# Kernel optimization log

Measured on AMD Instinct MI355X. Metric: run time of the kernel, lower is better.

Reference implementation:

```python
import jax, jax.numpy as jnp
import numpy as np

N = 50000   # nodes
E = 800000  # edges per relation (avg degree 16)
IN = 128    # input feature dim
H = 2       # attention heads per layer
OUT = 64    # output feats per head
R = 2       # number of relations
NEG_SLOPE = 0.2


def _edge_softmax(e, dst, n):
    # e: [E, H] edge scores; softmax over incoming edges of each dst node
    m = jax.ops.segment_max(e, dst, num_segments=n)  # [N, H]
    m = jnp.where(jnp.isfinite(m), m, 0.0)
    ex = jnp.exp(e - jax.lax.stop_gradient(m)[dst])
    s = jax.ops.segment_sum(ex, dst, num_segments=n)  # [N, H]
    return ex / s[dst]


def _gat_layer(h, W, al, ar, b, src, dst):
    # h: [N, in]; W: [R, in, H*OUT]; al/ar: [R, H, OUT]; b: [R, H*OUT]
    # src/dst: [R, E] int32. HeteroGraphConv with sum aggregation over relations.
    acc = jnp.zeros((N, H, OUT), h.dtype)
    for r in range(R):  # small fixed relation count
        f = (h @ W[r]).reshape(N, H, OUT)           # projected feats
        el = (f * al[r]).sum(-1)                    # [N, H]
        er = (f * ar[r]).sum(-1)                    # [N, H]
        e = jax.nn.leaky_relu(el[src[r]] + er[dst[r]], NEG_SLOPE)  # [E, H]
        a = _edge_softmax(e, dst[r], N)             # [E, H]
        msg = f[src[r]] * a[:, :, None]             # [E, H, OUT]
        agg = jax.ops.segment_sum(msg, dst[r], num_segments=N)     # [N, H, OUT]
        acc = acc + jax.nn.elu(agg + b[r].reshape(1, H, OUT))
    return acc.reshape(N, H * OUT)  # flatten(1)


def setup_inputs() -> dict:
    key = jax.random.key(0)
    k = jax.random.split(key, 13)
    s = 0.05
    f32 = jnp.float32
    return {
        "x": jax.random.normal(k[0], (N, IN), f32),
        "W0": jax.random.normal(k[1], (R, IN, H * OUT), f32) * s,
        "al0": jax.random.normal(k[2], (R, H, OUT), f32) * s,
        "ar0": jax.random.normal(k[3], (R, H, OUT), f32) * s,
        "b0": jax.random.normal(k[4], (R, H * OUT), f32) * s,
        "W1": jax.random.normal(k[5], (R, H * OUT, H * OUT), f32) * s,
        "al1": jax.random.normal(k[6], (R, H, OUT), f32) * s,
        "ar1": jax.random.normal(k[7], (R, H, OUT), f32) * s,
        "b1": jax.random.normal(k[8], (R, H * OUT), f32) * s,
        "src0": jax.random.randint(k[9], (R, E), 0, N, jnp.int32),
        "dst0": jax.random.randint(k[10], (R, E), 0, N, jnp.int32),
        "src1": jax.random.randint(k[11], (R, E), 0, N, jnp.int32),
        "dst1": jax.random.randint(k[12], (R, E), 0, N, jnp.int32),
    }


def reference(x, W0, al0, ar0, b0, W1, al1, ar1, b1, src0, dst0, src1, dst1):
    h = _gat_layer(x, W0, al0, ar0, b0, src0, dst0)  # [N, H*OUT]
    h = _gat_layer(h, W1, al1, ar1, b1, src1, dst1)  # [N, H*OUT]
    return h
```

## Files before the change

kernel.cpp:

```cpp
#include <hip/hip_runtime.h>

#define NN 50000
#define NE 800000
#define DIM 128
#define NB 128
#define CH 2048
#define CAP 8192
#define MAXDEG 64
#define WINH 196
#define BPSET ((NE + CH - 1) / CH)
#define NBIN_BLOCKS (4 * BPSET)
#define GRBLK ((NN + 63) / 64)
#define NGEMM (2 * GRBLK)

typedef unsigned int uint;
typedef unsigned short ushort;
typedef __attribute__((ext_vector_type(8))) short v8s;
typedef __attribute__((ext_vector_type(4))) float v4f;

__device__ __forceinline__ ushort f2bf(float f) {
    union { float f; uint i; } c; c.f = f;
    const uint r = (c.i + 0x7fffu + ((c.i >> 16) & 1u)) >> 16;
    return (ushort)r;
}

__device__ __forceinline__ void conv_body(
    const float* __restrict__ W0, const float* __restrict__ W1,
    ushort* __restrict__ WT, int bid)
{
    const int t = bid * 256 + threadIdx.x;
#pragma unroll
    for (int i = 0; i < 4; i++) {
        const int o = t * 4 + i;
        const int m = o >> 14, rem = o & 16383;
        const int nrow = rem >> 7, k = rem & 127;
        const float* src = (m < 2) ? (W0 + (size_t)m * 16384)
                                   : (W1 + (size_t)(m - 2) * 16384);
        WT[o] = f2bf(src[k * 128 + nrow]);
    }
}

__device__ __forceinline__ void gemm_rel_body(
    ushort (*tile)[136],
    const ushort* __restrict__ hbf, const float* __restrict__ xf,
    const ushort* __restrict__ WTr,
    const float* __restrict__ alr, const float* __restrict__ arr,
    ushort* __restrict__ fgr, float* __restrict__ elp, float* __restrict__ erp,
    int n, int is_f32, int rb)
{
    const int tid = threadIdx.x;
    const int w = tid >> 6, lane = tid & 63;
    const int quad = lane >> 4, l16 = lane & 15;
    const int row0 = rb * 64 + w * 16;

    int arow = row0 + l16;
    if (arow >= n) arow = n - 1;

    v8s afr[4];
    if (is_f32) {
        const float* ap = xf + (size_t)arow * DIM + quad * 8;
#pragma unroll
        for (int kt = 0; kt < 4; kt++) {
            const float4 a0 = *(const float4*)(ap + kt * 32);
            const float4 a1 = *(const float4*)(ap + kt * 32 + 4);
            ushort tmp[8] = { f2bf(a0.x), f2bf(a0.y), f2bf(a0.z), f2bf(a0.w),
                              f2bf(a1.x), f2bf(a1.y), f2bf(a1.z), f2bf(a1.w) };
            afr[kt] = *(const v8s*)tmp;
        }
    } else {
        const ushort* ap = hbf + (size_t)arow * DIM + quad * 8;
#pragma unroll
        for (int kt = 0; kt < 4; kt++) afr[kt] = *(const v8s*)(ap + kt * 32);
    }

    const ushort* bp = WTr + (size_t)l16 * DIM + quad * 8;
    v4f acc[8];
#pragma unroll
    for (int nt = 0; nt < 8; nt++) acc[nt] = (v4f)0.0f;
#pragma unroll
    for (int kt = 0; kt < 4; kt++) {
#pragma unroll
        for (int nt = 0; nt < 8; nt++) {
            const v8s b = *(const v8s*)(bp + (size_t)nt * 16 * DIM + kt * 32);
            acc[nt] = __builtin_amdgcn_mfma_f32_16x16x32_bf16(afr[kt], b, acc[nt], 0, 0, 0);
        }
    }

    float pel[4][2], per2[4][2];
#pragma unroll
    for (int r = 0; r < 4; r++)
        pel[r][0] = pel[r][1] = per2[r][0] = per2[r][1] = 0.f;
#pragma unroll
    for (int nt = 0; nt < 8; nt++) {
        const int col = nt * 16 + l16;
        const float av = alr[col], rv = arr[col];
        const int head = nt >> 2;
#pragma unroll
        for (int r = 0; r < 4; r++) {
            pel[r][head] += acc[nt][r] * av;
            per2[r][head] += acc[nt][r] * rv;
        }
    }
#pragma unroll
    for (int o = 1; o < 16; o <<= 1) {
#pragma unroll
        for (int r = 0; r < 4; r++) {
#pragma unroll
            for (int h = 0; h < 2; h++) {
                pel[r][h] += __shfl_xor(pel[r][h], o);
                per2[r][h] += __shfl_xor(per2[r][h], o);
            }
        }
    }
    if (l16 == 0) {
#pragma unroll
        for (int r = 0; r < 4; r++) {
            const int row = row0 + quad * 4 + r;
            if (row < n) {
#pragma unroll
                for (int h = 0; h < 2; h++) {
                    elp[row * 2 + h] = pel[r][h];
                    erp[row * 2 + h] = per2[r][h];
                }
            }
        }
    }

    const int lr0 = w * 16 + quad * 4;
#pragma unroll
    for (int nt = 0; nt < 8; nt++) {
        const int col = nt * 16 + l16;
#pragma unroll
        for (int r = 0; r < 4; r++)
            tile[lr0 + r][col] = f2bf(acc[nt][r]);
    }
    __syncthreads();
    const int srow = tid >> 2, ch = tid & 3;
    const int grow = rb * 64 + srow;
    if (grow < n) {
        const uint4* lp = (const uint4*)&tile[srow][ch * 32];
        uint4* gp = (uint4*)(fgr + (size_t)grow * DIM + ch * 32);
        gp[0] = lp[0];
        gp[1] = lp[1];
        gp[2] = lp[2];
        gp[3] = lp[3];
    }
}

__global__ __launch_bounds__(256) void gemm_rel(
    const ushort* __restrict__ hbf, const float* __restrict__ xf,
    const ushort* __restrict__ WT,
    const float* __restrict__ al, const float* __restrict__ ar,
    ushort* __restrict__ fg0, ushort* __restrict__ fg1,
    float* __restrict__ elb, int n, int is_f32)
{
    __shared__ ushort tile[64][136];
    const int rel = blockIdx.x & 1, rb = blockIdx.x >> 1;
    float* elp = elb + (size_t)rel * NN * 4;
    gemm_rel_body(tile, hbf, xf, WT + (size_t)rel * DIM * DIM,
                  al + rel * DIM, ar + rel * DIM,
                  rel ? fg1 : fg0, elp, elp + (size_t)NN * 2,
                  n, is_f32, rb);
}

__device__ __forceinline__ void bin_body(
    char* smem,
    const int* __restrict__ dst0, const int* __restrict__ dst1,
    const int* __restrict__ src0, const int* __restrict__ src1,
    int* __restrict__ gcur, uint* __restrict__ binned, int bid)
{
    int* hist  = (int*)smem;
    int* ebase = hist + NB;
    int* lcur  = ebase + NB;
    int* gbase = lcur + NB;
    int* sc    = gbase + NB;
    uint* stage = (uint*)(sc + NB);

    const int s = bid / BPSET, cb = bid - s * BPSET;
    const int* dstp = (s < 2) ? (dst0 + (size_t)s * NE) : (dst1 + (size_t)(s - 2) * NE);
    const int* srcp = (s < 2) ? (src0 + (size_t)s * NE) : (src1 + (size_t)(s - 2) * NE);
    const int e0 = cb * CH;
    const int t = threadIdx.x;

    if (t < NB) hist[t] = 0;
    __syncthreads();

    int myd[8], mys[8];
#pragma unroll
    for (int k = 0; k < 8; k++) {
        const int e = e0 + t + k * 256;
        if (e < NE) {
            const int d = dstp[e];
            myd[k] = d;
            mys[k] = srcp[e];
            atomicAdd(&hist[(d * NB) / NN], 1);
        } else myd[k] = -1;
    }
    __syncthreads();
    if (t < NB) sc[t] = hist[t];
    __syncthreads();
    for (int o = 1; o < NB; o <<= 1) {
        int tv = 0;
        if (t < NB && t >= o) tv = sc[t - o];
        __syncthreads();
        if (t < NB) sc[t] += tv;
        __syncthreads();
    }
    if (t < NB) {
        ebase[t] = sc[t] - hist[t];
        lcur[t]  = sc[t] - hist[t];
        gbase[t] = (s * NB + t) * CAP + atomicAdd(&gcur[s * NB + t], hist[t]);
    }
    __syncthreads();
#pragma unroll
    for (int k = 0; k < 8; k++) {
        if (myd[k] >= 0) {
            const int b = (myd[k] * NB) / NN;
            const int p = atomicAdd(&lcur[b], 1);
            stage[p] = ((uint)myd[k] << 16) | (uint)mys[k];
        }
    }
    __syncthreads();
    const int total = ebase[NB - 1] + hist[NB - 1];
    for (int i = t; i < total; i += 256) {
        const uint v = stage[i];
        const int b = ((int)(v >> 16) * NB) / NN;
        binned[gbase[b] + (i - ebase[b])] = v;
    }
}

__global__ __launch_bounds__(256) void prep_a(
    const float* __restrict__ W0, const float* __restrict__ W1,
    ushort* __restrict__ WT,
    const int* __restrict__ dst0, const int* __restrict__ dst1,
    const int* __restrict__ src0, const int* __restrict__ src1,
    int* __restrict__ gcur, uint* __restrict__ binned)
{
    __shared__ __align__(16) char smem[10752];
    const int bid = blockIdx.x;
    if (bid < 64) {
        conv_body(W0, W1, WT, bid);
    } else {
        bin_body(smem, dst0, dst1, src0, src1, gcur, binned, bid - 64);
    }
}

__device__ __forceinline__ void slot_body(
    char* smem, const int* __restrict__ gcur, const uint* __restrict__ binned,
    int* __restrict__ cnt, ushort* __restrict__ slots, int bid2)
{
    ushort* win = (ushort*)smem;
    int* lcur = (int*)(smem + WINH * MAXDEG * 2);
    const int s = bid2 >> 8, rem = bid2 & 255;
    const int b = rem >> 1, half = rem & 1;
    const int wb0 = (b * NN + NB - 1) / NB;
    int wb1 = ((b + 1) * NN + NB - 1) / NB;
    if (wb1 > NN) wb1 = NN;
    const int nb0 = wb0 + half * WINH;
    int nb1 = nb0 + WINH;
    if (nb1 > wb1) nb1 = wb1;
    if (nb0 >= nb1) return;
    const int nloc = nb1 - nb0;
    int fill = gcur[s * NB + b];
    if (fill > CAP) fill = CAP;
    const uint* bslot = binned + (size_t)(s * NB + b) * CAP;
    const int t = threadIdx.x;

    uint* wz = (uint*)win;
    for (int i = t; i < WINH * MAXDEG / 2; i += 256) wz[i] = 0;
    for (int i = t; i < nloc; i += 256) lcur[i] = 0;
    __syncthreads();
    for (int j = t; j < fill; j += 256) {
        const uint v = bslot[j];
        const int d = (int)(v >> 16) - nb0;
        if ((uint)d < (uint)nloc) {
            const int p = atomicAdd(&lcur[d], 1);
            if (p < MAXDEG) win[d * MAXDEG + p] = (ushort)(v & 0xffffu);
        }
    }
    __syncthreads();
    const uint4* wsrc = (const uint4*)win;
    uint4* wdst = (uint4*)(slots + ((size_t)s * NN + nb0) * MAXDEG);
    const int nq = nloc * (MAXDEG / 8);
    for (int i = t; i < nq; i += 256) wdst[i] = wsrc[i];
    for (int i = t; i < nloc; i += 256) {
        const int c = lcur[i];
        cnt[s * NN + nb0 + i] = c < MAXDEG ? c : MAXDEG;
    }
}

__global__ __launch_bounds__(256) void prep_b(
    const float* __restrict__ xf, const ushort* __restrict__ WT,
    const float* __restrict__ al, const float* __restrict__ ar,
    ushort* __restrict__ fg0, ushort* __restrict__ fg1,
    float* __restrict__ elb,
    const int* __restrict__ gcur, const uint* __restrict__ binned,
    int* __restrict__ cnt, ushort* __restrict__ slots)
{
    __shared__ __align__(16) char smem[25888];
    const int bid = blockIdx.x;
    if (bid < NGEMM) {
        const int rel = bid & 1, rb = bid >> 1;
        float* elp = elb + (size_t)rel * NN * 4;
        gemm_rel_body((ushort(*)[136])smem, nullptr, xf,
                      WT + (size_t)rel * DIM * DIM,
                      al + rel * DIM, ar + rel * DIM,
                      rel ? fg1 : fg0, elp, elp + (size_t)NN * 2,
                      NN, 1, rb);
    } else {
        slot_body(smem, gcur, binned, cnt, slots, bid - NGEMM);
    }
}

__device__ __forceinline__ float elu(float v) { return v > 0.f ? v : expm1f(v); }
__device__ __forceinline__ float2 bfpair(uint u) {
    union { uint i; float f; } lo, hi;
    lo.i = u << 16;
    hi.i = u & 0xffff0000u;
    return make_float2(lo.f, hi.f);
}

__global__ __launch_bounds__(256) void aggregate_dual(
    const int* __restrict__ cnt0, const ushort* __restrict__ sl0,
    const int* __restrict__ cnt1, const ushort* __restrict__ sl1,
    const float2* __restrict__ el0, const float2* __restrict__ er0,
    const float2* __restrict__ el1, const float2* __restrict__ er1,
    const ushort* __restrict__ fg0, const ushort* __restrict__ fg1,
    const float* __restrict__ bias0, const float* __restrict__ bias1,
    float* __restrict__ outf, ushort* __restrict__ outbf, int obf)
{
    __shared__ uint soff[4][64];
    __shared__ float wts[4][2][64];
    const int wv = (blockIdx.x * 256 + threadIdx.x) >> 6;
    if (wv >= NN) return;
    const int lane = threadIdx.x & 63;
    const int wid = threadIdx.x >> 6;

    const int* cnts[2] = {cnt0, cnt1};
    const ushort* sls[2] = {sl0, sl1};
    const float2* els[2] = {el0, el1};
    const float2* ers[2] = {er0, er1};
    const ushort* fgs[2] = {fg0, fg1};
    const float* biases[2] = {bias0, bias1};

    float oacc0 = 0.f, oacc1 = 0.f;

#pragma unroll
    for (int rel = 0; rel < 2; rel++) {
        const int deg = cnts[rel][wv];
        const float2 erd = ers[rel][wv];
        float2 acc = make_float2(0.f, 0.f);

        uint sof = 0;
        float ex0 = 0.f, ex1 = 0.f;
        if (lane < deg) {
            const int s = sls[rel][(size_t)wv * MAXDEG + lane];
            const float2 e = els[rel][s];
            float e0 = e.x + erd.x, e1 = e.y + erd.y;
            e0 = e0 > 0.f ? e0 : 0.2f * e0;
            e1 = e1 > 0.f ? e1 : 0.2f * e1;
            ex0 = __expf(e0);
            ex1 = __expf(e1);
            sof = (uint)s << 8;
        }
        float den0 = ex0, den1 = ex1;
        for (int o = 32; o > 0; o >>= 1) {
            den0 += __shfl_xor(den0, o);
            den1 += __shfl_xor(den1, o);
        }
        const float inv0 = 1.0f / den0, inv1 = 1.0f / den1;
        soff[wid][lane] = sof;
        wts[wid][0][lane] = ex0 * inv0;
        wts[wid][1][lane] = ex1 * inv1;
        const char* fgb = (const char*)fgs[rel] + lane * 4;
        const float* wrow = wts[wid][lane >> 5];
        const uint* sorow = soff[wid];
        const int dp = (deg + 15) & ~15;
        for (int tt = 0; tt < dp; tt += 16) {
            uint off[16];
            float wgt[16];
#pragma unroll
            for (int k = 0; k < 16; k++) {
                off[k] = sorow[tt + k];
                wgt[k] = wrow[tt + k];
            }
            uint u[16];
#pragma unroll
            for (int k = 0; k < 16; k++)
                u[k] = *(const uint*)(fgb + off[k]);
#pragma unroll
            for (int k = 0; k < 16; k++) {
                const float2 f = bfpair(u[k]);
                acc.x += f.x * wgt[k];
                acc.y += f.y * wgt[k];
            }
        }

        const float b0 = biases[rel][2 * lane], b1 = biases[rel][2 * lane + 1];
        oacc0 += elu(acc.x + b0);
        oacc1 += elu(acc.y + b1);
    }

    if (obf) {
        ushort tmp[2] = { f2bf(oacc0), f2bf(oacc1) };
        *(uint*)(outbf + (size_t)wv * DIM + 2 * lane) = *(const uint*)tmp;
    } else {
        float* op = outf + (size_t)wv * DIM + 2 * lane;
        op[0] = oacc0; op[1] = oacc1;
    }
}

extern "C" void kernel_launch(void* const* d_in, const int* in_sizes, int n_in,
                              void* d_out, int out_size, void* d_ws, size_t ws_size,
                              hipStream_t stream)
{
    const float* x   = (const float*)d_in[0];
    const float* W0  = (const float*)d_in[1];
    const float* al0 = (const float*)d_in[2];
    const float* ar0 = (const float*)d_in[3];
    const float* b0  = (const float*)d_in[4];
    const float* W1  = (const float*)d_in[5];
    const float* al1 = (const float*)d_in[6];
    const float* ar1 = (const float*)d_in[7];
    const float* b1  = (const float*)d_in[8];
    const int* src0 = (const int*)d_in[9];
    const int* dst0 = (const int*)d_in[10];
    const int* src1 = (const int*)d_in[11];
    const int* dst1 = (const int*)d_in[12];
    float* out = (float*)d_out;

    char* w = (char*)d_ws;
    auto alloc = [&](size_t bytes) {
        char* p = w; w += (bytes + 255) & ~(size_t)255; return p;
    };
    ushort* h1bf   = (ushort*)alloc((size_t)NN * DIM * 2);
    ushort* fg0    = (ushort*)alloc((size_t)NN * DIM * 2);
    ushort* fg1    = (ushort*)alloc((size_t)NN * DIM * 2);
    ushort* WT     = (ushort*)alloc((size_t)4 * DIM * DIM * 2);
    float*  elb    = (float*)alloc((size_t)8 * NN * 4);
    int*    cnt    = (int*)alloc((size_t)4 * NN * 4);
    ushort* slots  = (ushort*)alloc((size_t)4 * NN * MAXDEG * 2);
    uint*   binned = (uint*)alloc((size_t)4 * NB * CAP * 4);
    int*    gcur   = (int*)alloc((size_t)4 * NB * 4);

    const int ablocks = (NN * 64 + 255) / 256;

    hipMemsetAsync(gcur, 0, (size_t)4 * NB * 4, stream);
    prep_a<<<64 + NBIN_BLOCKS, 256, 0, stream>>>(
        W0, W1, WT, dst0, dst1, src0, src1, gcur, binned);
    prep_b<<<NGEMM + 4 * NB * 2, 256, 0, stream>>>(
        x, WT, al0, ar0, fg0, fg1, elb, gcur, binned, cnt, slots);

    for (int L = 0; L < 2; L++) {
        if (L) {
            gemm_rel<<<NGEMM, 256, 0, stream>>>(
                h1bf, nullptr, WT + (size_t)2 * DIM * DIM, al1, ar1,
                fg0, fg1, elb, NN, 0);
        }
        const float* b = L ? b1 : b0;
        const int es0 = L * 2, es1 = L * 2 + 1;
        float* el0p = elb;
        float* er0p = elb + (size_t)NN * 2;
        float* el1p = elb + (size_t)NN * 4;
        float* er1p = elb + (size_t)NN * 6;
        aggregate_dual<<<ablocks, 256, 0, stream>>>(
            cnt + (size_t)es0 * NN, slots + (size_t)es0 * NN * MAXDEG,
            cnt + (size_t)es1 * NN, slots + (size_t)es1 * NN * MAXDEG,
            (const float2*)el0p, (const float2*)er0p,
            (const float2*)el1p, (const float2*)er1p,
            fg0, fg1, b, b + DIM,
            L ? out : nullptr, L ? nullptr : h1bf, L ? 0 : 1);
    }
}
```

Before: 338.9 us.

## Scatter binned edges directly and split slot windows into quarters

```diff
diff --git a/kernel.cpp b/kernel.cpp
--- a/kernel.cpp
+++ b/kernel.cpp
@@ -4,12 +4,13 @@
 #define NE 800000
 #define DIM 128
 #define NB 128
-#define CH 2048
+#define CH 4096
 #define CAP 8192
 #define MAXDEG 64
-#define WINH 196
+#define WINQ 98
 #define BPSET ((NE + CH - 1) / CH)
 #define NBIN_BLOCKS (4 * BPSET)
+#define NSLOT_BLOCKS (4 * NB * 4)
 #define GRBLK ((NN + 63) / 64)
 #define NGEMM (2 * GRBLK)
 
@@ -164,18 +165,11 @@
 }
 
 __device__ __forceinline__ void bin_body(
-    char* smem,
+    int* hist, int* gbase_l, int* lcur,
     const int* __restrict__ dst0, const int* __restrict__ dst1,
     const int* __restrict__ src0, const int* __restrict__ src1,
     int* __restrict__ gcur, uint* __restrict__ binned, int bid)
 {
-    int* hist  = (int*)smem;
-    int* ebase = hist + NB;
-    int* lcur  = ebase + NB;
-    int* gbase = lcur + NB;
-    int* sc    = gbase + NB;
-    uint* stage = (uint*)(sc + NB);
-
     const int s = bid / BPSET, cb = bid - s * BPSET;
     const int* dstp = (s < 2) ? (dst0 + (size_t)s * NE) : (dst1 + (size_t)(s - 2) * NE);
     const int* srcp = (s < 2) ? (src0 + (size_t)s * NE) : (src1 + (size_t)(s - 2) * NE);
@@ -185,9 +179,9 @@
     if (t < NB) hist[t] = 0;
     __syncthreads();
 
-    int myd[8], mys[8];
-#pragma unroll
-    for (int k = 0; k < 8; k++) {
+    int myd[16], mys[16];
+#pragma unroll
+    for (int k = 0; k < 16; k++) {
         const int e = e0 + t + k * 256;
         if (e < NE) {
             const int d = dstp[e];
@@ -197,35 +191,20 @@
         } else myd[k] = -1;
     }
     __syncthreads();
-    if (t < NB) sc[t] = hist[t];
-    __syncthreads();
-    for (int o = 1; o < NB; o <<= 1) {
-        int tv = 0;
-        if (t < NB && t >= o) tv = sc[t - o];
-        __syncthreads();
-        if (t < NB) sc[t] += tv;
-        __syncthreads();
-    }
     if (t < NB) {
-        ebase[t] = sc[t] - hist[t];
-        lcur[t]  = sc[t] - hist[t];
-        gbase[t] = (s * NB + t) * CAP + atomicAdd(&gcur[s * NB + t], hist[t]);
-    }
-    __syncthreads();
-#pragma unroll
-    for (int k = 0; k < 8; k++) {
+        const int h = hist[t];
+        const int base = h ? atomicAdd(&gcur[s * NB + t], h) : 0;
+        gbase_l[t] = (s * NB + t) * CAP + base;
+        lcur[t] = 0;
+    }
+    __syncthreads();
+#pragma unroll
+    for (int k = 0; k < 16; k++) {
         if (myd[k] >= 0) {
             const int b = (myd[k] * NB) / NN;
             const int p = atomicAdd(&lcur[b], 1);
-            stage[p] = ((uint)myd[k] << 16) | (uint)mys[k];
-        }
-    }
-    __syncthreads();
-    const int total = ebase[NB - 1] + hist[NB - 1];
-    for (int i = t; i < total; i += 256) {
-        const uint v = stage[i];
-        const int b = ((int)(v >> 16) * NB) / NN;
-        binned[gbase[b] + (i - ebase[b])] = v;
+            binned[gbase_l[b] + p] = ((uint)myd[k] << 16) | (uint)mys[k];
+        }
     }
 }
 
@@ -236,12 +215,13 @@
     const int* __restrict__ src0, const int* __restrict__ src1,
     int* __restrict__ gcur, uint* __restrict__ binned)
 {
-    __shared__ __align__(16) char smem[10752];
+    __shared__ int hist[NB], gbase_l[NB], lcur[NB];
     const int bid = blockIdx.x;
     if (bid < 64) {
         conv_body(W0, W1, WT, bid);
     } else {
-        bin_body(smem, dst0, dst1, src0, src1, gcur, binned, bid - 64);
+        bin_body(hist, gbase_l, lcur, dst0, dst1, src0, src1,
+                 gcur, binned, bid - 64);
     }
 }
 
@@ -250,14 +230,14 @@
     int* __restrict__ cnt, ushort* __restrict__ slots, int bid2)
 {
     ushort* win = (ushort*)smem;
-    int* lcur = (int*)(smem + WINH * MAXDEG * 2);
-    const int s = bid2 >> 8, rem = bid2 & 255;
-    const int b = rem >> 1, half = rem & 1;
+    int* lcur = (int*)(smem + WINQ * MAXDEG * 2);
+    const int s = bid2 >> 9, rem = bid2 & 511;
+    const int b = rem >> 2, q = rem & 3;
     const int wb0 = (b * NN + NB - 1) / NB;
     int wb1 = ((b + 1) * NN + NB - 1) / NB;
     if (wb1 > NN) wb1 = NN;
-    const int nb0 = wb0 + half * WINH;
-    int nb1 = nb0 + WINH;
+    const int nb0 = wb0 + q * WINQ;
+    int nb1 = nb0 + WINQ;
     if (nb1 > wb1) nb1 = wb1;
     if (nb0 >= nb1) return;
     const int nloc = nb1 - nb0;
@@ -267,7 +247,7 @@
     const int t = threadIdx.x;
 
     uint* wz = (uint*)win;
-    for (int i = t; i < WINH * MAXDEG / 2; i += 256) wz[i] = 0;
+    for (int i = t; i < WINQ * MAXDEG / 2; i += 256) wz[i] = 0;
     for (int i = t; i < nloc; i += 256) lcur[i] = 0;
     __syncthreads();
     for (int j = t; j < fill; j += 256) {
@@ -297,7 +277,7 @@
     const int* __restrict__ gcur, const uint* __restrict__ binned,
     int* __restrict__ cnt, ushort* __restrict__ slots)
 {
-    __shared__ __align__(16) char smem[25888];
+    __shared__ __align__(16) char smem[17408];
     const int bid = blockIdx.x;
     if (bid < NGEMM) {
         const int rel = bid & 1, rb = bid >> 1;
@@ -448,7 +428,7 @@
     hipMemsetAsync(gcur, 0, (size_t)4 * NB * 4, stream);
     prep_a<<<64 + NBIN_BLOCKS, 256, 0, stream>>>(
         W0, W1, WT, dst0, dst1, src0, src1, gcur, binned);
-    prep_b<<<NGEMM + 4 * NB * 2, 256, 0, stream>>>(
+    prep_b<<<NGEMM + NSLOT_BLOCKS, 256, 0, stream>>>(
         x, WT, al0, ar0, fg0, fg1, elb, gcur, binned, cnt, slots);
 
     for (int L = 0; L < 2; L++) {
```

Result: slower. 353.0 us (+4.2%).
